# Kernel tuning notes

Hardware: AMD Instinct MI355X
Metric: run time of the kernel (lower is better)

## Reference

```python
import jax, jax.numpy as jnp
import numpy as np

B, T, NF, C, H, TOPK = 4, 8, 8192, 384, 12, 32
D = C // H
SCALE = D ** -0.5  # qk_scale=None -> head_dim**-0.5


def setup_inputs() -> dict:
    key = jax.random.key(0)
    ks = jax.random.split(key, 4)
    x = jax.random.normal(ks[0], (B, T + NF, C), jnp.float32)
    qs_w = jax.random.normal(ks[1], (T, C, C), jnp.float32) * (C ** -0.5)
    kv_w = jax.random.normal(ks[2], (C, 2 * C), jnp.float32) * (C ** -0.5)
    experts_w = jax.random.normal(ks[3], (T, C, C), jnp.float32) * (C ** -0.5)
    return {"x": x, "qs_w": qs_w, "kv_w": kv_w, "experts_w": experts_w}


def reference(x, qs_w, kv_w, experts_w):
    # x: [B, T+NF, C]; first T tokens are task tokens, rest are feature tokens
    feature = x[:, T:, :]                                          # [B,NF,C]
    kv = (feature @ kv_w).reshape(B, NF, 2, H, D)                  # out dim splits [2,H,D]
    k = kv[:, :, 0].transpose(0, 2, 1, 3)                          # [B,H,NF,D]
    v = kv[:, :, 1].transpose(0, 2, 1, 3)                          # [B,H,NF,D]
    # per-task query linears (no bias), one task token each
    q = jnp.einsum('btc,tco->bto', x[:, :T, :], qs_w)              # [B,T,C]
    q = q.reshape(B, T, H, D).transpose(0, 2, 1, 3)                # [B,H,T,D]
    attn = jnp.einsum('bhtd,bhnd->bhtn', q, k) * SCALE             # [B,H,T,NF]
    vals, idx = jax.lax.top_k(attn, TOPK)                          # [B,H,T,K]
    w = jax.nn.softmax(vals, axis=-1)                              # softmax over top-k only
    # attn_token = (scatter(topk softmax) @ v) == weighted gather of v rows
    v_g = jnp.take_along_axis(v[:, :, None], idx[..., None], axis=3)   # [B,H,T,K,D]
    attn_token = jnp.einsum('bhtk,bhtkd->bhtd', w, v_g)
    attn_token = attn_token.transpose(0, 2, 1, 3).reshape(B, T, C)     # [B,T,C]
    # gather raw feature tokens at top-k indices, weight, scatter into padded zeros
    fm = feature.reshape(B, NF, H, D).transpose(0, 2, 1, 3)        # [B,H,NF,D]
    f_g = jnp.take_along_axis(fm[:, :, None], idx[..., None], axis=3) * w[..., None]  # [B,H,T,K,D]
    bi = jnp.arange(B)[:, None, None, None]
    hi = jnp.arange(H)[None, :, None, None]
    ti = jnp.arange(T)[None, None, :, None]
    # topk indices are unique per row -> set is well-defined
    feature_pad = jnp.zeros((B, H, T, NF, D), x.dtype).at[bi, hi, ti, idx].set(f_g)
    feature_pad = feature_pad.transpose(0, 2, 3, 1, 4).reshape(B, T, NF, C)  # [B,T,NF,C]
    # per-task expert linears; einsum with ones weight == sum over tasks
    feature_out = jnp.einsum('btnc,tco->bno', feature_pad, experts_w)  # [B,NF,C]
    token_out = jnp.einsum('btc,tco->bto', attn_token, experts_w)      # [B,T,C]
    return jnp.concatenate([token_out, feature_out], axis=1)          # [B,T+NF,C]
```

## Files before the change

kernel.cpp:

```cpp
#include <hip/hip_runtime.h>
#include <hip/hip_bf16.h>
#include <math.h>

#define B 4
#define T 8
#define NF 8192
#define C 384
#define H 12
#define TOPK 32
#define D 32
#define STOT (T + NF)
#define R (H * T)
#define KSEL 48
#define SCALE 0.17677669529663687f

typedef unsigned int uint;
typedef unsigned short ushort;
typedef short bf16x8 __attribute__((ext_vector_type(8)));
typedef float f32x4 __attribute__((ext_vector_type(4)));
typedef float f32x2 __attribute__((ext_vector_type(2)));

__device__ __forceinline__ ushort bf16u(float a) {
  return __builtin_bit_cast(ushort, __float2bfloat16(a));
}

__device__ __forceinline__ ushort f32_key(float s) {
  uint kb = bf16u(s);
  kb ^= (kb & 0x8000u) ? 0xFFFFu : 0x8000u;
  return (ushort)kb;
}

__global__ __launch_bounds__(256) void ta_qproj_kernel(
    const float* __restrict__ x, const float* __restrict__ qs_w,
    float* __restrict__ q_part) {
  int t = blockIdx.x;
  int o0 = blockIdx.y * 64;
  int z = blockIdx.z;
  int tid = threadIdx.x;
  int o = tid & 63, ks = tid >> 6;
  __shared__ float xs[B][192];
  __shared__ float part[4][B][64];
  if (tid < 192) {
    int b = tid / 48, j4 = (tid % 48) * 4;
    *reinterpret_cast<float4*>(&xs[b][j4]) =
        *reinterpret_cast<const float4*>(x + ((size_t)b * STOT + t) * C + z * 192 + j4);
  }
  __syncthreads();
  float a0 = 0.f, a1 = 0.f, a2 = 0.f, a3 = 0.f;
  const float* w = qs_w + (size_t)t * C * C + (size_t)(z * 192 + ks * 48) * C + o0 + o;
#pragma unroll 8
  for (int c = 0; c < 48; ++c) {
    float wv = w[(size_t)c * C];
    int cj = ks * 48 + c;
    a0 += xs[0][cj] * wv;
    a1 += xs[1][cj] * wv;
    a2 += xs[2][cj] * wv;
    a3 += xs[3][cj] * wv;
  }
  part[ks][0][o] = a0; part[ks][1][o] = a1;
  part[ks][2][o] = a2; part[ks][3][o] = a3;
  __syncthreads();
  {
    int b = tid >> 6, oo = tid & 63;
    float s = part[0][b][oo] + part[1][b][oo] + part[2][b][oo] + part[3][b][oo];
    q_part[(((size_t)z * B + b) * T + t) * C + o0 + oo] = s;
  }
}

__global__ __launch_bounds__(384) void ta_fold_kernel(
    const float* __restrict__ q_part, const float* __restrict__ kv_w,
    float* __restrict__ qk_f32, ushort* __restrict__ qk_bf) {
  int b = blockIdx.x / H, h = blockIdx.x % H;
  int tid = threadIdx.x;
  __shared__ float kS[C][33];
  __shared__ float qh[T][D];
  if (tid < T * D) {
    int t = tid >> 5, d = tid & 31;
    qh[t][d] = q_part[((size_t)b * T + t) * C + h * D + d] +
               q_part[(((size_t)B + b) * T + t) * C + h * D + d];
  }
  for (int j = tid; j < C * 8; j += 384) {
    int c = j >> 3, d4 = (j & 7) * 4;
    float4 v = *reinterpret_cast<const float4*>(
        kv_w + (size_t)c * (2 * C) + h * D + d4);
    kS[c][d4 + 0] = v.x; kS[c][d4 + 1] = v.y;
    kS[c][d4 + 2] = v.z; kS[c][d4 + 3] = v.w;
  }
  __syncthreads();
  float acc[T] = {0.f, 0.f, 0.f, 0.f, 0.f, 0.f, 0.f, 0.f};
#pragma unroll
  for (int d = 0; d < D; ++d) {
    float kv = kS[tid][d];
#pragma unroll
    for (int t = 0; t < T; ++t) acc[t] += qh[t][d] * kv;
  }
#pragma unroll
  for (int t = 0; t < T; ++t) {
    size_t off = ((size_t)b * R + (size_t)h * T + t) * C + tid;
    float a = acc[t];
    qk_f32[off] = a;
    qk_bf[off] = bf16u(a);
  }
}

__global__ __launch_bounds__(256) void ta_scores_kernel(
    const float* __restrict__ x, const ushort* __restrict__ qk_bf,
    ushort* __restrict__ keys, float4* __restrict__ out4) {
  int b = blockIdx.y;
  int n0 = blockIdx.x * 64;
  int tid = threadIdx.x;
  int lane = tid & 63, w = tid >> 6;
  int row16 = lane & 15, kg = lane >> 4;
  __shared__ ushort fS[64][72];
  __shared__ ushort qS[96][72];
  f32x4 acc[6];
#pragma unroll
  for (int i = 0; i < 6; ++i) acc[i] = (f32x4){0.f, 0.f, 0.f, 0.f};

  {
    const int SL = (B * STOT * C / 4) / 512;
    int zbid = blockIdx.y * gridDim.x + blockIdx.x;
    float4 z = {0.f, 0.f, 0.f, 0.f};
    float4* dst = out4 + (size_t)zbid * SL;
    for (int j = tid; j < SL; j += 256) dst[j] = z;
  }

  const float* xb = x + ((size_t)b * STOT + T + n0) * C;
  const ushort* qb = qk_bf + (size_t)b * R * C;

  int frow = tid >> 2, fcg = (tid & 3) * 8;

#pragma unroll 1
  for (int c0 = 0; c0 < C; c0 += 32) {
    {
      const float* src = xb + (size_t)frow * C + c0 + fcg;
      float4 v0 = *reinterpret_cast<const float4*>(src);
      float4 v1 = *reinterpret_cast<const float4*>(src + 4);
      uint4 p;
      p.x = (uint)bf16u(v0.x) | ((uint)bf16u(v0.y) << 16);
      p.y = (uint)bf16u(v0.z) | ((uint)bf16u(v0.w) << 16);
      p.z = (uint)bf16u(v1.x) | ((uint)bf16u(v1.y) << 16);
      p.w = (uint)bf16u(v1.z) | ((uint)bf16u(v1.w) << 16);
      *reinterpret_cast<uint4*>(&fS[frow][fcg]) = p;
    }
#pragma unroll
    for (int s = 0; s < 2; ++s) {
      int u = tid + 256 * s;
      if (u < 384) {
        int row = u >> 2, cg = (u & 3) * 8;
        uint4 v = *reinterpret_cast<const uint4*>(qb + (size_t)row * C + c0 + cg);
        *reinterpret_cast<uint4*>(&qS[row][cg]) = v;
      }
    }
    __syncthreads();
    bf16x8 bfr = *reinterpret_cast<const bf16x8*>(&fS[w * 16 + row16][kg * 8]);
#pragma unroll
    for (int i = 0; i < 6; ++i) {
      bf16x8 afr = *reinterpret_cast<const bf16x8*>(&qS[i * 16 + row16][kg * 8]);
      acc[i] = __builtin_amdgcn_mfma_f32_16x16x32_bf16(afr, bfr, acc[i], 0, 0, 0);
    }
    __syncthreads();
  }
  int n = n0 + w * 16 + row16;
#pragma unroll
  for (int i = 0; i < 6; ++i) {
    int rbase = i * 16 + kg * 4;
#pragma unroll
    for (int reg = 0; reg < 4; ++reg) {
      keys[((size_t)b * R + rbase + reg) * NF + n] = f32_key(acc[i][reg] * SCALE);
    }
  }
}

__global__ __launch_bounds__(384) void ta_selres_kernel(
    const ushort* __restrict__ keys, const float* __restrict__ x,
    const float* __restrict__ qk_f32, float* __restrict__ w_buf,
    int* __restrict__ idx_buf) {
  int rr = blockIdx.x;
  int b = rr / R;
  int tid = threadIdx.x;
  int lane = tid & 63, wvi = tid >> 6;
  __shared__ __align__(16) ushort su[NF];
  __shared__ uint hist[4096];
  __shared__ uint cand[1024];
  __shared__ uint wtot[4];
  __shared__ uint sh_piv, sh_above, cnt;
  __shared__ int il[KSEL];
  __shared__ float sv[KSEL];
  __shared__ int rkS[KSEL];
  __shared__ float qS[C];
  __shared__ float smax, esum;

  {
    const uint4* src = reinterpret_cast<const uint4*>(keys + (size_t)rr * NF);
    uint4* dst = reinterpret_cast<uint4*>(su);
    for (int j = tid; j < NF / 8; j += 384) dst[j] = src[j];
  }
  qS[tid] = qk_f32[(size_t)rr * C + tid];
  for (int i = tid; i < 4096; i += 384) hist[i] = 0;
  if (tid == 0) cnt = 0;
  __syncthreads();

  for (int i = tid; i < NF; i += 384) atomicAdd(&hist[su[i] >> 4], 1u);
  __syncthreads();

  uint pp = 0, suf = 0;
  if (tid < 256) {
#pragma unroll
    for (int j = 0; j < 16; ++j) pp += hist[tid * 16 + j];
    suf = pp;
#pragma unroll
    for (int off = 1; off < 64; off <<= 1) {
      uint o = __shfl_down(suf, off);
      if (lane + off < 64) suf += o;
    }
    if (lane == 0) wtot[wvi] = suf;
  }
  __syncthreads();
  if (tid < 256) {
    uint later = 0;
    for (int wq = wvi + 1; wq < 4; ++wq) later += wtot[wq];
    uint geg = later + suf;
    uint gng = geg - pp;
    if (geg >= (uint)KSEL && gng < (uint)KSEL) {
      uint run = gng;
      int pv = 0; uint ab = 0;
      for (int j = 15; j >= 0; --j) {
        uint c = hist[tid * 16 + j];
        uint nrun = run + c;
        if (nrun >= (uint)KSEL && run < (uint)KSEL) { pv = tid * 16 + j; ab = run; }
        run = nrun;
      }
      sh_piv = (uint)pv; sh_above = ab;
    }
  }
  __syncthreads();
  uint piv = sh_piv;
  for (int i = tid; i < NF; i += 384) {
    uint u = su[i];
    if ((u >> 4) >= piv) {
      uint s = atomicAdd(&cnt, 1u);
      if (s < 1024) cand[s] = (u << 13) | (8191u - (uint)i);
    }
  }
  __syncthreads();
  {
    uint m = cnt < 1024u ? cnt : 1024u;
    if (tid < (int)m) {
      uint me = cand[tid];
      int r = 0;
      for (uint e = 0; e < m; ++e) r += (cand[e] > me);
      if (r < KSEL) il[r] = 8191 - (int)(me & 8191u);
    }
  }
  __syncthreads();

  int k = tid >> 3, j = tid & 7;
  const float* fp = x + ((size_t)b * STOT + T + il[k]) * C + j;
  float s = 0.f;
#pragma unroll 8
  for (int m2 = 0; m2 < 48; ++m2) s += fp[m2 * 8] * qS[j + m2 * 8];
  s += __shfl_down(s, 4);
  s += __shfl_down(s, 2);
  s += __shfl_down(s, 1);
  if (j == 0) sv[k] = s * SCALE;
  __syncthreads();
  if (tid < KSEL) {
    float mys = sv[tid];
    int myn = il[tid];
    int r = 0;
#pragma unroll
    for (int e = 0; e < KSEL; ++e) {
      float se = sv[e];
      r += (se > mys) || (se == mys && il[e] < myn);
    }
    rkS[tid] = r;
    if (r == 0) smax = mys;
  }
  __syncthreads();
  float e = 0.f;
  if (tid < KSEL && rkS[tid] < TOPK) e = expf(sv[tid] - smax);
  if (tid < 64) {
    float t2 = e;
#pragma unroll
    for (int off = 32; off; off >>= 1) t2 += __shfl_down(t2, off);
    if (tid == 0) esum = t2;
  }
  __syncthreads();
  if (tid < KSEL && rkS[tid] < TOPK) {
    w_buf[(size_t)rr * TOPK + rkS[tid]] = e / esum;
    idx_buf[(size_t)rr * TOPK + rkS[tid]] = il[tid];
  }
}

__global__ __launch_bounds__(256) void ta_gvscatter_kernel(
    const float* __restrict__ x, const float* __restrict__ kv_w,
    const float* __restrict__ ew, const float* __restrict__ w_buf,
    const int* __restrict__ idx_buf, float* __restrict__ out) {
  constexpr int KH = TOPK / 2;
  int br = blockIdx.x >> 1, half = blockIdx.x & 1;
  int t = br % T, h = (br / T) % H, b = br / R;
  int tid = threadIdx.x;
  int k16 = tid >> 4, lane16 = tid & 15, d0 = 2 * lane16;
  __shared__ float Fc[KH][100];
  __shared__ float Vc[96][36];
  __shared__ float vS[KH][36];
  __shared__ float gS[KH][36];
  __shared__ __align__(16) float attS[D];
  __shared__ float wl[KH];
  __shared__ int il[KH];

  if (tid < KH) {
    wl[tid] = w_buf[(size_t)br * TOPK + half * KH + tid];
    il[tid] = idx_buf[(size_t)br * TOPK + half * KH + tid];
  }
  __syncthreads();
  f32x2 acc = {0.f, 0.f};
  int hc = (h * D) / 96;
#pragma unroll 1
  for (int ch = 0; ch < 4; ++ch) {
    int c0 = ch * 96;
    if (ch) __syncthreads();
#pragma unroll
    for (int s = 0; s < 2; ++s) {
      int u = tid + 256 * s;
      if (u < 384) {
        int kr = u / 24, c4 = (u % 24) * 4;
        *reinterpret_cast<float4*>(&Fc[kr][c4]) =
            *reinterpret_cast<const float4*>(
                x + ((size_t)b * STOT + T + il[kr]) * C + c0 + c4);
      }
    }
#pragma unroll
    for (int s = 0; s < 3; ++s) {
      int u = tid + 256 * s;
      int cr = u >> 3, d4 = (u & 7) * 4;
      *reinterpret_cast<float4*>(&Vc[cr][d4]) =
          *reinterpret_cast<const float4*>(
              kv_w + (size_t)(c0 + cr) * (2 * C) + C + h * D + d4);
    }
    __syncthreads();
    if (ch == hc) {
      int off = h * D - c0;
      f32x2 f = *reinterpret_cast<const f32x2*>(&Fc[k16][off + d0]);
      float wk = wl[k16];
      gS[k16][d0] = wk * f.x;
      gS[k16][d0 + 1] = wk * f.y;
    }
#pragma unroll 4
    for (int c = 0; c < 96; c += 4) {
      float4 f4 = *reinterpret_cast<const float4*>(&Fc[k16][c]);
      f32x2 v0 = *reinterpret_cast<const f32x2*>(&Vc[c + 0][d0]);
      f32x2 v1 = *reinterpret_cast<const f32x2*>(&Vc[c + 1][d0]);
      f32x2 v2 = *reinterpret_cast<const f32x2*>(&Vc[c + 2][d0]);
      f32x2 v3 = *reinterpret_cast<const f32x2*>(&Vc[c + 3][d0]);
      acc.x += f4.x * v0.x + f4.y * v1.x + f4.z * v2.x + f4.w * v3.x;
      acc.y += f4.x * v0.y + f4.y * v1.y + f4.z * v2.y + f4.w * v3.y;
    }
  }
  vS[k16][d0] = acc.x;
  vS[k16][d0 + 1] = acc.y;
  __syncthreads();
  if (tid < D) {
    float a = 0.f;
#pragma unroll
    for (int kk = 0; kk < KH; ++kk) a += wl[kk] * vS[kk][tid];
    attS[tid] = a;
  }
  __syncthreads();

  float ewc0[D], ewc1[D];
  const float* ewt = ew + (size_t)t * C * C + (size_t)h * D * C;
#pragma unroll
  for (int dd = 0; dd < D; ++dd) {
    ewc0[dd] = ewt[(size_t)dd * C + tid];
    ewc1[dd] = (tid < 128) ? ewt[(size_t)dd * C + tid + 256] : 0.f;
  }
  size_t obase = (size_t)b * STOT * C;
#pragma unroll 1
  for (int kk = 0; kk < KH; ++kk) {
    float y0 = 0.f, y1 = 0.f;
#pragma unroll
    for (int d4 = 0; d4 < D; d4 += 4) {
      float4 g4 = *reinterpret_cast<const float4*>(&gS[kk][d4]);
      y0 += g4.x * ewc0[d4] + g4.y * ewc0[d4 + 1] +
            g4.z * ewc0[d4 + 2] + g4.w * ewc0[d4 + 3];
      y1 += g4.x * ewc1[d4] + g4.y * ewc1[d4 + 1] +
            g4.z * ewc1[d4 + 2] + g4.w * ewc1[d4 + 3];
    }
    size_t row = obase + (size_t)(T + il[kk]) * C;
    atomicAdd(&out[row + tid], y0);
    if (tid < 128) atomicAdd(&out[row + tid + 256], y1);
  }
  {
    float y0 = 0.f, y1 = 0.f;
#pragma unroll
    for (int d4 = 0; d4 < D; d4 += 4) {
      float4 a4 = *reinterpret_cast<const float4*>(attS + d4);
      y0 += a4.x * ewc0[d4] + a4.y * ewc0[d4 + 1] +
            a4.z * ewc0[d4 + 2] + a4.w * ewc0[d4 + 3];
      y1 += a4.x * ewc1[d4] + a4.y * ewc1[d4 + 1] +
            a4.z * ewc1[d4 + 2] + a4.w * ewc1[d4 + 3];
    }
    size_t row = obase + (size_t)t * C;
    atomicAdd(&out[row + tid], y0);
    if (tid < 128) atomicAdd(&out[row + tid + 256], y1);
  }
}

extern "C" void kernel_launch(void* const* d_in, const int* in_sizes, int n_in,
                              void* d_out, int out_size, void* d_ws, size_t ws_size,
                              hipStream_t stream) {
  const float* x = (const float*)d_in[0];
  const float* qs_w = (const float*)d_in[1];
  const float* kv_w = (const float*)d_in[2];
  const float* ew = (const float*)d_in[3];
  float* out = (float*)d_out;

  char* p = (char*)d_ws;
  float* qk_f32 = (float*)p;  p += (size_t)B * R * C * 4;
  ushort* qk_bf = (ushort*)p; p += (size_t)B * R * C * 2;
  ushort* keys = (ushort*)p;  p += (size_t)B * R * NF * 2;
  float* w_buf = (float*)p;   p += (size_t)B * R * TOPK * 4;
  int* idx_buf = (int*)p;     p += (size_t)B * R * TOPK * 4;
  float* q_part = (float*)p;

  dim3 gq(T, C / 64, 2);
  ta_qproj_kernel<<<gq, 256, 0, stream>>>(x, qs_w, q_part);
  ta_fold_kernel<<<B * H, 384, 0, stream>>>(q_part, kv_w, qk_f32, qk_bf);
  dim3 g2(NF / 64, B);
  ta_scores_kernel<<<g2, 256, 0, stream>>>(x, qk_bf, keys, (float4*)out);
  ta_selres_kernel<<<B * R, 384, 0, stream>>>(keys, x, qk_f32, w_buf, idx_buf);
  ta_gvscatter_kernel<<<B * R * 2, 256, 0, stream>>>(x, kv_w, ew, w_buf, idx_buf, out);
}
```

Measured before the change: 87.64 us.

## Reassociate weighted V gather as weighted feature sum times kv_w slice

```diff
diff --git a/kernel.cpp b/kernel.cpp
--- a/kernel.cpp
+++ b/kernel.cpp
@@ -18,7 +18,6 @@
 typedef unsigned short ushort;
 typedef short bf16x8 __attribute__((ext_vector_type(8)));
 typedef float f32x4 __attribute__((ext_vector_type(4)));
-typedef float f32x2 __attribute__((ext_vector_type(2)));
 
 __device__ __forceinline__ ushort bf16u(float a) {
   return __builtin_bit_cast(ushort, __float2bfloat16(a));
@@ -293,7 +292,7 @@
   }
 }
 
-__global__ __launch_bounds__(256) void ta_gvscatter_kernel(
+__global__ __launch_bounds__(384) void ta_gvscatter_kernel(
     const float* __restrict__ x, const float* __restrict__ kv_w,
     const float* __restrict__ ew, const float* __restrict__ w_buf,
     const int* __restrict__ idx_buf, float* __restrict__ out) {
@@ -301,110 +300,80 @@
   int br = blockIdx.x >> 1, half = blockIdx.x & 1;
   int t = br % T, h = (br / T) % H, b = br / R;
   int tid = threadIdx.x;
-  int k16 = tid >> 4, lane16 = tid & 15, d0 = 2 * lane16;
-  __shared__ float Fc[KH][100];
-  __shared__ float Vc[96][36];
-  __shared__ float vS[KH][36];
-  __shared__ float gS[KH][36];
-  __shared__ __align__(16) float attS[D];
+  int hD = h * D;
   __shared__ float wl[KH];
   __shared__ int il[KH];
+  __shared__ float fbarS[C];
+  __shared__ float gS[KH][D];
+  __shared__ float part[8][D];
+  __shared__ __align__(16) float attS[D];
 
   if (tid < KH) {
     wl[tid] = w_buf[(size_t)br * TOPK + half * KH + tid];
     il[tid] = idx_buf[(size_t)br * TOPK + half * KH + tid];
   }
   __syncthreads();
-  f32x2 acc = {0.f, 0.f};
-  int hc = (h * D) / 96;
-#pragma unroll 1
-  for (int ch = 0; ch < 4; ++ch) {
-    int c0 = ch * 96;
-    if (ch) __syncthreads();
-#pragma unroll
-    for (int s = 0; s < 2; ++s) {
-      int u = tid + 256 * s;
-      if (u < 384) {
-        int kr = u / 24, c4 = (u % 24) * 4;
-        *reinterpret_cast<float4*>(&Fc[kr][c4]) =
-            *reinterpret_cast<const float4*>(
-                x + ((size_t)b * STOT + T + il[kr]) * C + c0 + c4);
-      }
-    }
-#pragma unroll
-    for (int s = 0; s < 3; ++s) {
-      int u = tid + 256 * s;
-      int cr = u >> 3, d4 = (u & 7) * 4;
-      *reinterpret_cast<float4*>(&Vc[cr][d4]) =
-          *reinterpret_cast<const float4*>(
-              kv_w + (size_t)(c0 + cr) * (2 * C) + C + h * D + d4);
-    }
-    __syncthreads();
-    if (ch == hc) {
-      int off = h * D - c0;
-      f32x2 f = *reinterpret_cast<const f32x2*>(&Fc[k16][off + d0]);
-      float wk = wl[k16];
-      gS[k16][d0] = wk * f.x;
-      gS[k16][d0 + 1] = wk * f.y;
-    }
+
+  {
+    float fbar = 0.f;
+    bool ing = (tid >= hD) && (tid < hD + D);
 #pragma unroll 4
-    for (int c = 0; c < 96; c += 4) {
-      float4 f4 = *reinterpret_cast<const float4*>(&Fc[k16][c]);
-      f32x2 v0 = *reinterpret_cast<const f32x2*>(&Vc[c + 0][d0]);
-      f32x2 v1 = *reinterpret_cast<const f32x2*>(&Vc[c + 1][d0]);
-      f32x2 v2 = *reinterpret_cast<const f32x2*>(&Vc[c + 2][d0]);
-      f32x2 v3 = *reinterpret_cast<const f32x2*>(&Vc[c + 3][d0]);
-      acc.x += f4.x * v0.x + f4.y * v1.x + f4.z * v2.x + f4.w * v3.x;
-      acc.y += f4.x * v0.y + f4.y * v1.y + f4.z * v2.y + f4.w * v3.y;
-    }
-  }
-  vS[k16][d0] = acc.x;
-  vS[k16][d0 + 1] = acc.y;
+    for (int k = 0; k < KH; ++k) {
+      float v = x[((size_t)b * STOT + T + il[k]) * C + tid];
+      float wv = wl[k] * v;
+      fbar += wv;
+      if (ing) gS[k][tid - hD] = wv;
+    }
+    fbarS[tid] = fbar;
+  }
+  __syncthreads();
+
+  if (tid < 256) {
+    int d = tid & 31, seg = tid >> 5;
+    const float* vw = kv_w + C + hD + d;
+    float a0 = 0.f, a1 = 0.f;
+    int cb = seg * 48;
+#pragma unroll 8
+    for (int c = 0; c < 48; c += 2) {
+      a0 += fbarS[cb + c] * vw[(size_t)(cb + c) * (2 * C)];
+      a1 += fbarS[cb + c + 1] * vw[(size_t)(cb + c + 1) * (2 * C)];
+    }
+    part[seg][d] = a0 + a1;
+  }
   __syncthreads();
   if (tid < D) {
     float a = 0.f;
 #pragma unroll
-    for (int kk = 0; kk < KH; ++kk) a += wl[kk] * vS[kk][tid];
+    for (int s = 0; s < 8; ++s) a += part[s][tid];
     attS[tid] = a;
   }
   __syncthreads();
 
-  float ewc0[D], ewc1[D];
-  const float* ewt = ew + (size_t)t * C * C + (size_t)h * D * C;
-#pragma unroll
-  for (int dd = 0; dd < D; ++dd) {
-    ewc0[dd] = ewt[(size_t)dd * C + tid];
-    ewc1[dd] = (tid < 128) ? ewt[(size_t)dd * C + tid + 256] : 0.f;
-  }
-  size_t obase = (size_t)b * STOT * C;
+  float ewc[D];
+  const float* ewt = ew + (size_t)t * C * C + (size_t)hD * C + tid;
+#pragma unroll
+  for (int dd = 0; dd < D; ++dd) ewc[dd] = ewt[(size_t)dd * C];
+  size_t obase = (size_t)b * STOT * C + tid;
 #pragma unroll 1
   for (int kk = 0; kk < KH; ++kk) {
-    float y0 = 0.f, y1 = 0.f;
+    float y = 0.f;
 #pragma unroll
     for (int d4 = 0; d4 < D; d4 += 4) {
       float4 g4 = *reinterpret_cast<const float4*>(&gS[kk][d4]);
-      y0 += g4.x * ewc0[d4] + g4.y * ewc0[d4 + 1] +
-            g4.z * ewc0[d4 + 2] + g4.w * ewc0[d4 + 3];
-      y1 += g4.x * ewc1[d4] + g4.y * ewc1[d4 + 1] +
-            g4.z * ewc1[d4 + 2] + g4.w * ewc1[d4 + 3];
-    }
-    size_t row = obase + (size_t)(T + il[kk]) * C;
-    atomicAdd(&out[row + tid], y0);
-    if (tid < 128) atomicAdd(&out[row + tid + 256], y1);
-  }
-  {
-    float y0 = 0.f, y1 = 0.f;
+      y += g4.x * ewc[d4] + g4.y * ewc[d4 + 1] +
+           g4.z * ewc[d4 + 2] + g4.w * ewc[d4 + 3];
+    }
+    atomicAdd(&out[obase + (size_t)(T + il[kk]) * C], y);
+  }
+  {
+    float y = 0.f;
 #pragma unroll
     for (int d4 = 0; d4 < D; d4 += 4) {
       float4 a4 = *reinterpret_cast<const float4*>(attS + d4);
-      y0 += a4.x * ewc0[d4] + a4.y * ewc0[d4 + 1] +
-            a4.z * ewc0[d4 + 2] + a4.w * ewc0[d4 + 3];
-      y1 += a4.x * ewc1[d4] + a4.y * ewc1[d4 + 1] +
-            a4.z * ewc1[d4 + 2] + a4.w * ewc1[d4 + 3];
-    }
-    size_t row = obase + (size_t)t * C;
-    atomicAdd(&out[row + tid], y0);
-    if (tid < 128) atomicAdd(&out[row + tid + 256], y1);
+      y += a4.x * ewc[d4] + a4.y * ewc[d4 + 1] +
+           a4.z * ewc[d4 + 2] + a4.w * ewc[d4 + 3];
+    }
+    atomicAdd(&out[obase + (size_t)t * C], y);
   }
 }
 
@@ -431,5 +400,5 @@
   dim3 g2(NF / 64, B);
   ta_scores_kernel<<<g2, 256, 0, stream>>>(x, qk_bf, keys, (float4*)out);
   ta_selres_kernel<<<B * R, 384, 0, stream>>>(keys, x, qk_f32, w_buf, idx_buf);
-  ta_gvscatter_kernel<<<B * R * 2, 256, 0, stream>>>(x, kv_w, ew, w_buf, idx_buf, out);
-}
+  ta_gvscatter_kernel<<<B * R * 2, 384, 0, stream>>>(x, kv_w, ew, w_buf, idx_buf, out);
+}
```

Result: faster. 80.48 us (-8.2%).
